# Performance work log

Hardware: AMD Instinct MI355X
Metric: run time of the kernel (lower is better)

The kernel has to match this reference:

```python
import jax, jax.numpy as jnp
import numpy as np

N_LAYERS = 200
KSIZE = 7
L_IN = 1388
FC_IN = 188   # 1388 - 200*6
FC_OUT = 91


def setup_inputs() -> dict:
    key = jax.random.key(0)
    k_x, k_w, k_b, k_fw, k_fb = jax.random.split(key, 5)
    B = 1024
    x = jax.random.normal(k_x, (B, L_IN), dtype=jnp.float32)
    # Conv1d(1,1,7) weights: torch default init U(-s, s) with s = 1/sqrt(in_ch*k) = 1/sqrt(7)
    s = 1.0 / np.sqrt(KSIZE)
    conv_w = jax.random.uniform(k_w, (N_LAYERS, KSIZE), dtype=jnp.float32, minval=-s, maxval=s)
    conv_b = jax.random.uniform(k_b, (N_LAYERS,), dtype=jnp.float32, minval=-s, maxval=s)
    sf = 1.0 / np.sqrt(FC_IN)
    fc_w = jax.random.uniform(k_fw, (FC_OUT, FC_IN), dtype=jnp.float32, minval=-sf, maxval=sf)
    fc_b = jax.random.uniform(k_fb, (FC_OUT,), dtype=jnp.float32, minval=-sf, maxval=sf)
    return {"x": x, "conv_w": conv_w, "conv_b": conv_b, "fc_w": fc_w, "fc_b": fc_b}


def _conv1(h, w, b):
    # h: [B, L]; cross-correlation with taps w[0..6], valid padding -> [B, L-6]
    L_out = h.shape[1] - (KSIZE - 1)
    acc = w[0] * h[:, 0:L_out]
    for k in range(1, KSIZE):
        acc = acc + w[k] * h[:, k:k + L_out]
    return acc + b


def reference(x, conv_w, conv_b, fc_w, fc_b):
    h = x  # unsqueeze(1) is implicit: single channel handled as [B, L]
    for i in range(N_LAYERS):
        h = _conv1(h, conv_w[i], conv_b[i])
        if i < N_LAYERS - 1:  # last ReLU was popped in the torch module
            h = jax.nn.relu(h)
    # Linear(188, 91) applied to the length dim, then Sigmoid; squeeze channel dim
    out = jax.nn.sigmoid(h @ fc_w.T + fc_b)  # [B, 91]
    return out
```

## Files before the change

kernel.cpp:

```cpp
#include <hip/hip_runtime.h>
#include <math.h>

#define N_LAYERS 200
#define KSIZE 7
#define L_IN 1388
#define FC_IN 188
#define FC_OUT 91
#define NT 128
#define RMAX 12
#define NSTAGES 13

constexpr int s_lo(int s)  { return 16 * s; }
constexpr int s_hi(int s)  { return (s < 12) ? 16 * s + 16 : N_LAYERS; }
constexpr int lin_(int s)  { return L_IN - 6 * s_lo(s); }
constexpr int lout_(int s) { return L_IN - 6 * s_hi(s); }
constexpr int cut_(int s)  { return lout_(s) / 2; }
constexpr int marg_(int s) { return 6 * (s_hi(s) - s_lo(s)); }
constexpr int s_R(int s) {
    const int a = cut_(s) + marg_(s);
    const int b = lin_(s) - cut_(s);
    const int m = (a > b) ? a : b;
    return (m + 63) / 64;
}

__device__ __forceinline__ float dpp_next(float v) {
    return __int_as_float(
        __builtin_amdgcn_mov_dpp(__float_as_int(v), 0x130, 0xf, 0xf, true));
}

struct WG { float w[28]; float b[4]; };

__device__ __forceinline__ void load_wg(WG& wg, const float4* __restrict__ cw4,
                                        const float4* __restrict__ cb4, int g) {
#pragma unroll
    for (int t = 0; t < 7; ++t) {
        const float4 v = cw4[g * 7 + t];
        wg.w[4 * t + 0] = v.x; wg.w[4 * t + 1] = v.y;
        wg.w[4 * t + 2] = v.z; wg.w[4 * t + 3] = v.w;
    }
    const float4 bv = cb4[g];
    wg.b[0] = bv.x; wg.b[1] = bv.y; wg.b[2] = bv.z; wg.b[3] = bv.w;
}

template<int R, bool NR3>
__device__ __forceinline__ void run4(float (&r)[RMAX], const WG& wg) {
    constexpr int T1N = (R < 6) ? R : 6;
    constexpr int T2N = (R < 6) ? (6 - R) : 0;
#pragma unroll
    for (int j = 0; j < 4; ++j) {
        float t1[T1N];
#pragma unroll
        for (int t = 0; t < T1N; ++t) t1[t] = dpp_next(r[t]);
        float t2[T2N ? T2N : 1];
        if constexpr (T2N > 0) {
#pragma unroll
            for (int u = 0; u < T2N; ++u) t2[u] = dpp_next(t1[u]);
        }

        float acc[R];
#pragma unroll
        for (int d = 0; d < KSIZE; ++d) {
            const float wd = wg.w[j * 7 + d];
#pragma unroll
            for (int k = 0; k < R; ++k) {
                const int m = k + d;
                const float v = (m < R) ? r[m]
                              : ((m - R < T1N) ? t1[m - R] : t2[m - 2 * R]);
                acc[k] = (d == 0) ? fmaf(wd, v, wg.b[j]) : fmaf(wd, v, acc[k]);
            }
        }

        const bool relu = !(NR3 && j == 3);
#pragma unroll
        for (int k = 0; k < R; ++k)
            r[k] = relu ? fmaxf(acc[k], 0.0f) : acc[k];
    }
}

template<int R, bool FINAL>
__device__ __forceinline__ void run_stage_g(float (&r)[RMAX], WG& A,
        const float4* __restrict__ cw4, const float4* __restrict__ cb4,
        int g0, int g1) {
#pragma unroll 1
    for (int g = g0; g < g1; g += 2) {
        WG B;
        load_wg(B, cw4, cb4, (g + 1 < 50) ? g + 1 : 49);
        run4<R, false>(r, A);
        load_wg(A, cw4, cb4, (g + 2 < 50) ? g + 2 : 49);
        run4<R, FINAL>(r, B);
    }
}

template<int Ro, int Rn>
__device__ __forceinline__ void repack(float (&r)[RMAX], float* lbuf,
                                       int lane, int wid,
                                       int cut_o, int lout_o, int cut_n)
{
    const int base_o = wid ? cut_o : 0;
    const int bound  = wid ? lout_o : cut_o;
#pragma unroll
    for (int k = 0; k < Ro; ++k) {
        const int g = base_o + lane * Ro + k;
        if (g < bound) lbuf[g] = r[k];
    }
    __syncthreads();
    const int base_n = wid ? cut_n : 0;
#pragma unroll
    for (int k = 0; k < Rn; ++k) r[k] = lbuf[base_n + lane * Rn + k];
    __syncthreads();
}

template<int S>
struct Chain {
    __device__ static __forceinline__ void run(float (&r)[RMAX], WG& A,
        const float4* __restrict__ cw4, const float4* __restrict__ cb4,
        float* lbuf, int lane, int wid)
    {
        run_stage_g<s_R(S), false>(r, A, cw4, cb4, 4 * S, 4 * S + 4);
        repack<s_R(S), s_R(S + 1)>(r, lbuf, lane, wid,
                                   cut_(S), lout_(S), cut_(S + 1));
        Chain<S + 1>::run(r, A, cw4, cb4, lbuf, lane, wid);
    }
};

template<>
struct Chain<NSTAGES - 1> {
    __device__ static __forceinline__ void run(float (&r)[RMAX], WG& A,
        const float4* __restrict__ cw4, const float4* __restrict__ cb4,
        float* lbuf, int lane, int wid)
    {
        constexpr int R = s_R(NSTAGES - 1);
        run_stage_g<R, true>(r, A, cw4, cb4, 48, 50);
        const int base_o = wid ? 94 : 0;
        const int bound  = wid ? FC_IN : 94;
#pragma unroll
        for (int k = 0; k < R; ++k) {
            const int g = base_o + lane * R + k;
            if (g < bound) lbuf[g] = r[k];
        }
        __syncthreads();
    }
};

__global__ __launch_bounds__(NT, 2) void conv_chain_kernel(
    const float* __restrict__ x,
    const float* __restrict__ conv_w,
    const float* __restrict__ conv_b,
    const float* __restrict__ fc_w,
    const float* __restrict__ fc_b,
    float* __restrict__ out)
{
    __shared__ __align__(16) float lbuf[1312];

    const int row  = blockIdx.x;
    const int tid  = threadIdx.x;
    const int lane = tid & 63;
    const int wid  = tid >> 6;

    const float4* cw4 = (const float4*)conv_w;
    const float4* cb4 = (const float4*)conv_b;

    WG A;
    load_wg(A, cw4, cb4, 0);

    float r[RMAX];
    const float* xr = x + (size_t)row * L_IN;
    constexpr int R0 = s_R(0);
    const int c0 = wid ? cut_(0) : 0;
#pragma unroll
    for (int k = 0; k < R0; ++k) {
        const int p = c0 + lane * R0 + k;
        r[k] = (p < L_IN) ? xr[p] : 0.0f;
    }

    Chain<0>::run(r, A, cw4, cb4, lbuf, lane, wid);

    if (tid < FC_OUT) {
        float acc = fc_b[tid];
        const float4* wp = (const float4*)(fc_w + tid * FC_IN);
        const float4* hp = (const float4*)lbuf;
#pragma unroll 4
        for (int q = 0; q < FC_IN / 4; ++q) {
            const float4 hv = hp[q];
            const float4 wv = wp[q];
            acc = fmaf(wv.x, hv.x, acc);
            acc = fmaf(wv.y, hv.y, acc);
            acc = fmaf(wv.z, hv.z, acc);
            acc = fmaf(wv.w, hv.w, acc);
        }
        out[(size_t)row * FC_OUT + tid] = 1.0f / (1.0f + expf(-acc));
    }
}

extern "C" void kernel_launch(void* const* d_in, const int* in_sizes, int n_in,
                              void* d_out, int out_size, void* d_ws, size_t ws_size,
                              hipStream_t stream) {
    const float* x      = (const float*)d_in[0];
    const float* conv_w = (const float*)d_in[1];
    const float* conv_b = (const float*)d_in[2];
    const float* fc_w   = (const float*)d_in[3];
    const float* fc_b   = (const float*)d_in[4];
    float* outp = (float*)d_out;

    const int batch = in_sizes[0] / L_IN;
    conv_chain_kernel<<<batch, NT, 0, stream>>>(x, conv_w, conv_b, fc_w, fc_b, outp);
}
```

Before: 119.6 us.

## Use packed FP32 FMA over register pairs and stage conv weights in LDS

Switches the per-thread register window from scalar floats to pairs of floats, so the conv taps run with packed two-wide FMA/max operations. Odd-offset taps use shuffled pair vectors. Conv weights and biases are broadcast into duplicated pairs in shared memory at kernel start, and per-group weight loads now read from LDS instead of global memory. The aim is to halve the VALU instruction count of the conv chain. The cost is extra register shuffles, a larger LDS footprint that may reduce occupancy, and an upfront weight-staging pass per block.

```diff
diff --git a/kernel.cpp b/kernel.cpp
--- a/kernel.cpp
+++ b/kernel.cpp
@@ -7,8 +7,9 @@
 #define FC_IN 188
 #define FC_OUT 91
 #define NT 128
-#define RMAX 12
 #define NSTAGES 13
+
+typedef float v2f __attribute__((ext_vector_type(2)));
 
 constexpr int s_lo(int s)  { return 16 * s; }
 constexpr int s_hi(int s)  { return (s < 12) ? 16 * s + 16 : N_LAYERS; }
@@ -22,121 +23,133 @@
     const int m = (a > b) ? a : b;
     return (m + 63) / 64;
 }
+constexpr int s_Re(int s) { return (s_R(s) + 1) & ~1; }
 
 __device__ __forceinline__ float dpp_next(float v) {
     return __int_as_float(
         __builtin_amdgcn_mov_dpp(__float_as_int(v), 0x130, 0xf, 0xf, true));
 }
-
-struct WG { float w[28]; float b[4]; };
-
-__device__ __forceinline__ void load_wg(WG& wg, const float4* __restrict__ cw4,
-                                        const float4* __restrict__ cb4, int g) {
-#pragma unroll
-    for (int t = 0; t < 7; ++t) {
-        const float4 v = cw4[g * 7 + t];
-        wg.w[4 * t + 0] = v.x; wg.w[4 * t + 1] = v.y;
-        wg.w[4 * t + 2] = v.z; wg.w[4 * t + 3] = v.w;
-    }
-    const float4 bv = cb4[g];
-    wg.b[0] = bv.x; wg.b[1] = bv.y; wg.b[2] = bv.z; wg.b[3] = bv.w;
+__device__ __forceinline__ v2f dpp_next2(v2f v) {
+    v2f o; o.x = dpp_next(v.x); o.y = dpp_next(v.y); return o;
+}
+
+__device__ __forceinline__ v2f pk_fma(v2f a, v2f b, v2f c) {
+    return __builtin_elementwise_fma(a, b, c);
+}
+__device__ __forceinline__ v2f pk_max0(v2f a) {
+    return __builtin_elementwise_max(a, (v2f)(0.0f));
+}
+
+struct WG { v2f w2[28]; v2f b2[4]; };
+
+__device__ __forceinline__ void load_wg(WG& wg, const v2f* wbuf2,
+                                        const v2f* bbuf2, int g) {
+#pragma unroll
+    for (int t = 0; t < 28; ++t) wg.w2[t] = wbuf2[g * 28 + t];
+#pragma unroll
+    for (int j = 0; j < 4; ++j) wg.b2[j] = bbuf2[g * 4 + j];
 }
 
 template<int R, bool NR3>
-__device__ __forceinline__ void run4(float (&r)[RMAX], const WG& wg) {
-    constexpr int T1N = (R < 6) ? R : 6;
-    constexpr int T2N = (R < 6) ? (6 - R) : 0;
-#pragma unroll
-    for (int j = 0; j < 4; ++j) {
-        float t1[T1N];
-#pragma unroll
-        for (int t = 0; t < T1N; ++t) t1[t] = dpp_next(r[t]);
-        float t2[T2N ? T2N : 1];
-        if constexpr (T2N > 0) {
-#pragma unroll
-            for (int u = 0; u < T2N; ++u) t2[u] = dpp_next(t1[u]);
-        }
-
-        float acc[R];
-#pragma unroll
-        for (int d = 0; d < KSIZE; ++d) {
-            const float wd = wg.w[j * 7 + d];
-#pragma unroll
-            for (int k = 0; k < R; ++k) {
-                const int m = k + d;
-                const float v = (m < R) ? r[m]
-                              : ((m - R < T1N) ? t1[m - R] : t2[m - 2 * R]);
-                acc[k] = (d == 0) ? fmaf(wd, v, wg.b[j]) : fmaf(wd, v, acc[k]);
+__device__ __forceinline__ void run4(v2f (&r2)[6], const WG& wg) {
+    constexpr int P = R / 2;
+#pragma unroll
+    for (int jj = 0; jj < 4; ++jj) {
+        v2f h[3];
+        {
+            constexpr int L1 = (P < 3) ? P : 3;
+            v2f l1[L1];
+#pragma unroll
+            for (int t = 0; t < L1; ++t) l1[t] = dpp_next2(r2[t]);
+#pragma unroll
+            for (int t = 0; t < L1; ++t) h[t] = l1[t];
+            if constexpr (P == 2) h[2] = dpp_next2(l1[0]);
+        }
+        v2f M[P + 2];
+#pragma unroll
+        for (int j = 0; j < P + 2; ++j) {
+            const v2f a = (j < P) ? r2[j] : h[j - P];
+            const v2f b = (j + 1 < P) ? r2[j + 1] : h[j + 1 - P];
+            v2f m; m.x = a.y; m.y = b.x;
+            M[j] = m;
+        }
+        const bool relu = !(NR3 && jj == 3);
+#pragma unroll
+        for (int j = 0; j < P; ++j) {
+            v2f acc = wg.b2[jj];
+#pragma unroll
+            for (int d = 0; d < KSIZE; ++d) {
+                v2f src;
+                if (d % 2 == 0) {
+                    const int m = j + d / 2;
+                    src = (m < P) ? r2[m] : h[m - P];
+                } else {
+                    src = M[j + (d - 1) / 2];
+                }
+                acc = pk_fma(wg.w2[jj * 7 + d], src, acc);
             }
-        }
-
-        const bool relu = !(NR3 && j == 3);
-#pragma unroll
-        for (int k = 0; k < R; ++k)
-            r[k] = relu ? fmaxf(acc[k], 0.0f) : acc[k];
+            r2[j] = relu ? pk_max0(acc) : acc;
+        }
     }
 }
 
 template<int R, bool FINAL>
-__device__ __forceinline__ void run_stage_g(float (&r)[RMAX], WG& A,
-        const float4* __restrict__ cw4, const float4* __restrict__ cb4,
-        int g0, int g1) {
+__device__ __forceinline__ void run_stage_g(v2f (&r2)[6], WG& A,
+        const v2f* wbuf2, const v2f* bbuf2, int g0, int g1) {
 #pragma unroll 1
     for (int g = g0; g < g1; g += 2) {
         WG B;
-        load_wg(B, cw4, cb4, (g + 1 < 50) ? g + 1 : 49);
-        run4<R, false>(r, A);
-        load_wg(A, cw4, cb4, (g + 2 < 50) ? g + 2 : 49);
-        run4<R, FINAL>(r, B);
+        load_wg(B, wbuf2, bbuf2, (g + 1 < 50) ? g + 1 : 49);
+        run4<R, false>(r2, A);
+        load_wg(A, wbuf2, bbuf2, (g + 2 < 50) ? g + 2 : 49);
+        run4<R, FINAL>(r2, B);
     }
 }
 
 template<int Ro, int Rn>
-__device__ __forceinline__ void repack(float (&r)[RMAX], float* lbuf,
+__device__ __forceinline__ void repack(v2f (&r2)[6], v2f* lbuf2,
                                        int lane, int wid,
                                        int cut_o, int lout_o, int cut_n)
 {
-    const int base_o = wid ? cut_o : 0;
-    const int bound  = wid ? lout_o : cut_o;
-#pragma unroll
-    for (int k = 0; k < Ro; ++k) {
-        const int g = base_o + lane * Ro + k;
-        if (g < bound) lbuf[g] = r[k];
+    const int base2  = (wid ? cut_o : 0) / 2;
+    const int bound2 = (wid ? lout_o : cut_o) / 2;
+#pragma unroll
+    for (int j = 0; j < Ro / 2; ++j) {
+        const int pg = base2 + lane * (Ro / 2) + j;
+        if (pg < bound2) lbuf2[pg] = r2[j];
     }
     __syncthreads();
-    const int base_n = wid ? cut_n : 0;
-#pragma unroll
-    for (int k = 0; k < Rn; ++k) r[k] = lbuf[base_n + lane * Rn + k];
+    const int nb2 = (wid ? cut_n : 0) / 2;
+#pragma unroll
+    for (int j = 0; j < Rn / 2; ++j) r2[j] = lbuf2[nb2 + lane * (Rn / 2) + j];
     __syncthreads();
 }
 
 template<int S>
 struct Chain {
-    __device__ static __forceinline__ void run(float (&r)[RMAX], WG& A,
-        const float4* __restrict__ cw4, const float4* __restrict__ cb4,
-        float* lbuf, int lane, int wid)
+    __device__ static __forceinline__ void run(v2f (&r2)[6], WG& A,
+        const v2f* wbuf2, const v2f* bbuf2, v2f* lbuf2, int lane, int wid)
     {
-        run_stage_g<s_R(S), false>(r, A, cw4, cb4, 4 * S, 4 * S + 4);
-        repack<s_R(S), s_R(S + 1)>(r, lbuf, lane, wid,
-                                   cut_(S), lout_(S), cut_(S + 1));
-        Chain<S + 1>::run(r, A, cw4, cb4, lbuf, lane, wid);
+        run_stage_g<s_Re(S), false>(r2, A, wbuf2, bbuf2, 4 * S, 4 * S + 4);
+        repack<s_Re(S), s_Re(S + 1)>(r2, lbuf2, lane, wid,
+                                     cut_(S), lout_(S), cut_(S + 1));
+        Chain<S + 1>::run(r2, A, wbuf2, bbuf2, lbuf2, lane, wid);
     }
 };
 
 template<>
 struct Chain<NSTAGES - 1> {
-    __device__ static __forceinline__ void run(float (&r)[RMAX], WG& A,
-        const float4* __restrict__ cw4, const float4* __restrict__ cb4,
-        float* lbuf, int lane, int wid)
+    __device__ static __forceinline__ void run(v2f (&r2)[6], WG& A,
+        const v2f* wbuf2, const v2f* bbuf2, v2f* lbuf2, int lane, int wid)
     {
-        constexpr int R = s_R(NSTAGES - 1);
-        run_stage_g<R, true>(r, A, cw4, cb4, 48, 50);
-        const int base_o = wid ? 94 : 0;
-        const int bound  = wid ? FC_IN : 94;
-#pragma unroll
-        for (int k = 0; k < R; ++k) {
-            const int g = base_o + lane * R + k;
-            if (g < bound) lbuf[g] = r[k];
+        constexpr int R = s_Re(NSTAGES - 1);
+        run_stage_g<R, true>(r2, A, wbuf2, bbuf2, 48, 50);
+        const int base2  = wid ? 47 : 0;
+        const int bound2 = wid ? 94 : 47;
+#pragma unroll
+        for (int j = 0; j < R / 2; ++j) {
+            const int pg = base2 + lane * (R / 2) + j;
+            if (pg < bound2) lbuf2[pg] = r2[j];
         }
         __syncthreads();
     }
@@ -150,35 +163,47 @@
     const float* __restrict__ fc_b,
     float* __restrict__ out)
 {
-    __shared__ __align__(16) float lbuf[1312];
+    __shared__ __align__(16) v2f lbuf2[688];
+    __shared__ __align__(16) v2f wbuf2[N_LAYERS * KSIZE];
+    __shared__ __align__(16) v2f bbuf2[N_LAYERS];
 
     const int row  = blockIdx.x;
     const int tid  = threadIdx.x;
     const int lane = tid & 63;
     const int wid  = tid >> 6;
 
-    const float4* cw4 = (const float4*)conv_w;
-    const float4* cb4 = (const float4*)conv_b;
+    for (int i = tid; i < N_LAYERS * KSIZE; i += NT) {
+        const float v = conv_w[i];
+        v2f p; p.x = v; p.y = v; wbuf2[i] = p;
+    }
+    for (int i = tid; i < N_LAYERS; i += NT) {
+        const float v = conv_b[i];
+        v2f p; p.x = v; p.y = v; bbuf2[i] = p;
+    }
+
+    v2f r2[6];
+    const float* xr = x + (size_t)row * L_IN;
+    const int c0 = wid ? cut_(0) : 0;
+#pragma unroll
+    for (int j = 0; j < 6; ++j) {
+        const int p = c0 + lane * 12 + 2 * j;
+        v2f v;
+        if (p + 1 < L_IN)      v = *(const v2f*)(xr + p);
+        else if (p < L_IN)     { v.x = xr[p]; v.y = 0.0f; }
+        else                   { v.x = 0.0f;  v.y = 0.0f; }
+        r2[j] = v;
+    }
+    __syncthreads();
 
     WG A;
-    load_wg(A, cw4, cb4, 0);
-
-    float r[RMAX];
-    const float* xr = x + (size_t)row * L_IN;
-    constexpr int R0 = s_R(0);
-    const int c0 = wid ? cut_(0) : 0;
-#pragma unroll
-    for (int k = 0; k < R0; ++k) {
-        const int p = c0 + lane * R0 + k;
-        r[k] = (p < L_IN) ? xr[p] : 0.0f;
-    }
-
-    Chain<0>::run(r, A, cw4, cb4, lbuf, lane, wid);
+    load_wg(A, wbuf2, bbuf2, 0);
+
+    Chain<0>::run(r2, A, wbuf2, bbuf2, lbuf2, lane, wid);
 
     if (tid < FC_OUT) {
         float acc = fc_b[tid];
         const float4* wp = (const float4*)(fc_w + tid * FC_IN);
-        const float4* hp = (const float4*)lbuf;
+        const float4* hp = (const float4*)lbuf2;
 #pragma unroll 4
         for (int q = 0; q < FC_IN / 4; ++q) {
             const float4 hv = hp[q];
```

Result: faster. 115.0 us (-3.9%).
